# Performance work log

Measured on AMD Instinct MI355X. Metric: run time of the kernel, lower is better.

## Reference

```python
import jax, jax.numpy as jnp
import numpy as np

B, S, D, H, MEL = 64, 512, 512, 8, 80
HD = D // H  # head dim


def _lstm_cell(x, h, c, w_ih, w_hh, b_ih, b_hh):
    # torch gate order: i, f, g, o
    gates = x @ w_ih.T + h @ w_hh.T + b_ih + b_hh
    i, f, g, o = jnp.split(gates, 4, axis=-1)
    c = jax.nn.sigmoid(f) * c + jax.nn.sigmoid(i) * jnp.tanh(g)
    h = jax.nn.sigmoid(o) * jnp.tanh(c)
    return h, c


def setup_inputs() -> dict:
    key = jax.random.key(0)
    ks = jax.random.split(key, 24)
    s = 0.05
    inp = {"encoder_output": jax.random.normal(ks[0], (B, S, D), jnp.float32)}
    # MultiheadAttention params (torch layout: in_proj [3D, D])
    inp["attn_in_w"] = jax.random.normal(ks[1], (3 * D, D), jnp.float32) * s
    inp["attn_in_b"] = jax.random.normal(ks[2], (3 * D,), jnp.float32) * s
    inp["attn_out_w"] = jax.random.normal(ks[3], (D, D), jnp.float32) * s
    inp["attn_out_b"] = jax.random.normal(ks[4], (D,), jnp.float32) * s
    # LSTM1 (2 layers)
    names = [("l1_w_ih0", (4 * D, D)), ("l1_w_hh0", (4 * D, D)), ("l1_b_ih0", (4 * D,)), ("l1_b_hh0", (4 * D,)),
             ("l1_w_ih1", (4 * D, D)), ("l1_w_hh1", (4 * D, D)), ("l1_b_ih1", (4 * D,)), ("l1_b_hh1", (4 * D,)),
             ("l2_w_ih", (4 * D, D)), ("l2_w_hh", (4 * D, D)), ("l2_b_ih", (4 * D,)), ("l2_b_hh", (4 * D,)),
             ("proj_w", (MEL, D)), ("proj_b", (MEL,))]
    for i, (n, shp) in enumerate(names):
        inp[n] = jax.random.normal(ks[5 + i], shp, jnp.float32) * s
    return inp


def reference(encoder_output, attn_in_w, attn_in_b, attn_out_w, attn_out_b,
              l1_w_ih0, l1_w_hh0, l1_b_ih0, l1_b_hh0,
              l1_w_ih1, l1_w_hh1, l1_b_ih1, l1_b_hh1,
              l2_w_ih, l2_w_hh, l2_b_ih, l2_b_hh, proj_w, proj_b):
    b, s, d = encoder_output.shape
    max_len = s * 5
    wq, wk, wv = jnp.split(attn_in_w, 3, axis=0)
    bq, bk, bv = jnp.split(attn_in_b, 3, axis=0)
    # Precompute K, V over encoder output: [B, S, H, HD]
    K = (encoder_output @ wk.T + bk).reshape(b, s, H, HD)
    V = (encoder_output @ wv.T + bv).reshape(b, s, H, HD)
    scale = 1.0 / np.sqrt(HD)

    def attend(x):  # x: [B, D] single-token query
        q = ((x @ wq.T + bq) * scale).reshape(b, H, HD)
        scores = jnp.einsum('bhd,bshd->bhs', q, K)
        w = jax.nn.softmax(scores, axis=-1)
        ctx = jnp.einsum('bhs,bshd->bhd', w, V).reshape(b, d)
        return ctx @ attn_out_w.T + attn_out_b

    zeros = jnp.zeros((b, d), encoder_output.dtype)
    carry0 = (zeros, zeros, zeros, zeros, zeros, zeros, zeros)

    def step(carry, _):
        h10, c10, h11, c11, h2, c2, dec_in = carry
        h10, c10 = _lstm_cell(dec_in, h10, c10, l1_w_ih0, l1_w_hh0, l1_b_ih0, l1_b_hh0)
        h11, c11 = _lstm_cell(h10, h11, c11, l1_w_ih1, l1_w_hh1, l1_b_ih1, l1_b_hh1)
        attn_out = attend(h11)
        h2, c2 = _lstm_cell(attn_out, h2, c2, l2_w_ih, l2_w_hh, l2_b_ih, l2_b_hh)
        out = h2 @ proj_w.T + proj_b  # [B, MEL]
        return (h10, c10, h11, c11, h2, c2, h2), out

    _, ys = jax.lax.scan(step, carry0, None, length=max_len)
    return jnp.transpose(ys, (1, 0, 2))  # [B, max_len, MEL]
```

## Files before the change

kernel.cpp:

```cpp
#include <hip/hip_runtime.h>
#include <hip/hip_bf16.h>
#include <hip/hip_fp8.h>

#define DEV_INLINE __device__ __forceinline__

typedef __attribute__((ext_vector_type(8))) short bf16x8;
typedef __attribute__((ext_vector_type(4))) float f32x4;
typedef __attribute__((ext_vector_type(2))) float f32x2;
typedef __attribute__((ext_vector_type(4))) unsigned int u32x4;
typedef unsigned long long ull;

constexpr int Bc = 64, Sc = 512, Dc = 512, Hc = 8, HDc = 64, MELc = 80, Tc = 2560;
constexpr int OUTSTRIDE = Tc * MELc;

constexpr size_t SZ_KP8 = 64ull * 8 * 512 * 64;
constexpr size_t SZ_VP  = 64ull * 8 * 512 * 64 * 2;
constexpr size_t SZ_PL  = 128ull * 2048 * 16;
constexpr size_t OFF_KP8 = 0;
constexpr size_t OFF_VP  = OFF_KP8 + SZ_KP8;
constexpr size_t OFF_PL0 = OFF_VP + SZ_VP;
constexpr size_t OFF_PL1 = OFF_PL0 + SZ_PL;
constexpr size_t OFF_PL2 = OFF_PL1 + SZ_PL;
constexpr size_t OFF_PWQ = OFF_PL2 + SZ_PL;
constexpr size_t OFF_PP  = OFF_PWQ + 524288;
constexpr size_t OFF_BL0 = OFF_PP + 81920;
constexpr size_t OFF_BL1 = OFF_BL0 + 8192;
constexpr size_t OFF_BL2 = OFF_BL1 + 8192;
constexpr size_t OFF_B2E = OFF_BL2 + 8192;
constexpr size_t OFF_W2E = OFF_B2E + 8192;
constexpr size_t OFF_WOT = OFF_W2E + 2097152;
constexpr size_t OFF_ACT = OFF_WOT + 1048576;
constexpr size_t OFF_FLG = OFF_ACT + 524288;

constexpr unsigned DYN_LDS = 137344;

DEV_INLINE float bf2f(short s) { return __uint_as_float(((unsigned)(unsigned short)s) << 16); }
DEV_INLINE short f2bf(float f) { union { __hip_bfloat16 h; short s; } u; u.h = __float2bfloat16(f); return u.s; }
DEV_INLINE float sig_f(float x) { return 1.0f / (1.0f + __expf(-x)); }
DEV_INLINE float tanh_f(float x) {
  float ax = fabsf(x);
  float e = __expf(fminf(2.0f * ax, 80.0f));
  float r = 1.0f - 2.0f / (e + 1.0f);
  return copysignf(r, x);
}
DEV_INLINE bf16x8 cvt8(const float* p) {
  bf16x8 r;
#pragma unroll
  for (int i = 0; i < 8; ++i) r[i] = f2bf(p[i]);
  return r;
}
DEV_INLINE float fp8tof(unsigned v) {
  __hip_fp8_e4m3 t; t.__x = (__hip_fp8_storage_t)v; return (float)t;
}

template <bool HI>
DEV_INLINE f32x2 cvt2_fp8(unsigned w) {
#if defined(__has_builtin) && __has_builtin(__builtin_amdgcn_cvt_pk_f32_fp8)
  return __builtin_amdgcn_cvt_pk_f32_fp8(w, HI);
#else
  unsigned b = HI ? (w >> 16) : w;
  f32x2 r; r[0] = fp8tof(b & 0xFFu); r[1] = fp8tof((b >> 8) & 0xFFu);
  return r;
#endif
}

DEV_INLINE ull ld_dev_u64(const void* p) {
  return __hip_atomic_load((const ull*)p, __ATOMIC_RELAXED, __HIP_MEMORY_SCOPE_AGENT);
}
DEV_INLINE void st_dev_u64(void* p, ull v) {
  __hip_atomic_store((ull*)p, v, __ATOMIC_RELAXED, __HIP_MEMORY_SCOPE_AGENT);
}
DEV_INLINE bf16x8 ld_frag(const __hip_bfloat16* p) {
  union { bf16x8 v; ull u[2]; } r;
  r.u[0] = ld_dev_u64(p);
  r.u[1] = ld_dev_u64((const char*)p + 8);
  return r.v;
}

__global__ __launch_bounds__(256) void gemm_setup(const float* __restrict__ A,
                                                  const float* __restrict__ Bt,
                                                  const float* __restrict__ bias,
                                                  __hip_bfloat16* __restrict__ dst,
                                                  unsigned char* __restrict__ dst8,
                                                  int mode) {
  int tid = threadIdx.x, lane = tid & 63, wv = tid >> 6;
  int m0 = blockIdx.y * 64 + wv * 16;
  int nb = blockIdx.x * 64;
  int mrow = m0 + (lane & 15);
  int kb = (lane >> 4) * 8;
  f32x4 acc0 = {0,0,0,0}, acc1 = {0,0,0,0}, acc2 = {0,0,0,0}, acc3 = {0,0,0,0};
  const float* arow = A + (size_t)mrow * 512 + kb;
  const float* b0r = Bt + (size_t)(nb + 0 * 16 + (lane & 15)) * 512 + kb;
  const float* b1r = Bt + (size_t)(nb + 1 * 16 + (lane & 15)) * 512 + kb;
  const float* b2r = Bt + (size_t)(nb + 2 * 16 + (lane & 15)) * 512 + kb;
  const float* b3r = Bt + (size_t)(nb + 3 * 16 + (lane & 15)) * 512 + kb;
  for (int kk = 0; kk < 16; ++kk) {
    bf16x8 af = cvt8(arow + kk * 32);
    acc0 = __builtin_amdgcn_mfma_f32_16x16x32_bf16(af, cvt8(b0r + kk * 32), acc0, 0, 0, 0);
    acc1 = __builtin_amdgcn_mfma_f32_16x16x32_bf16(af, cvt8(b1r + kk * 32), acc1, 0, 0, 0);
    acc2 = __builtin_amdgcn_mfma_f32_16x16x32_bf16(af, cvt8(b2r + kk * 32), acc2, 0, 0, 0);
    acc3 = __builtin_amdgcn_mfma_f32_16x16x32_bf16(af, cvt8(b3r + kk * 32), acc3, 0, 0, 0);
  }
  int col16 = lane & 15, r0 = (lane >> 4) * 4;
  f32x4 accs[4] = {acc0, acc1, acc2, acc3};
#pragma unroll
  for (int nt = 0; nt < 4; ++nt) {
    int n = nb + nt * 16 + col16;
#pragma unroll
    for (int r = 0; r < 4; ++r) {
      int m = m0 + r0 + r;
      float v = accs[nt][r];
      if (mode == 0) {
        v += bias[n];
        int bb = m >> 9, s = m & 511, h = n >> 6, d = n & 63;
        dst[(((size_t)(bb * 8 + h) * 512 + s) * 64) + d] = __float2bfloat16(v);
      } else if (mode == 2) {
        v += bias[n];
        int bb = m >> 9, s = m & 511, h = n >> 6, d = n & 63;
        __hip_fp8_e4m3 q(v);
        dst8[(((size_t)(bb * 8 + h) * 512 + s) * 64) + d] = (unsigned char)q.__x;
      } else {
        dst[(size_t)m * 512 + n] = __float2bfloat16(v);
      }
    }
  }
}

__global__ __launch_bounds__(256) void transpose512(const float* __restrict__ in, float* __restrict__ out) {
  __shared__ float tl[32][33];
  int x = threadIdx.x & 31, ty = threadIdx.x >> 5;
  int bx = blockIdx.x * 32, by = blockIdx.y * 32;
#pragma unroll
  for (int r = 0; r < 4; ++r) tl[ty + r * 8][x] = in[(size_t)(by + ty + r * 8) * 512 + bx + x];
  __syncthreads();
#pragma unroll
  for (int r = 0; r < 4; ++r) out[(size_t)(bx + ty + r * 8) * 512 + by + x] = tl[x][ty + r * 8];
}

__global__ __launch_bounds__(256) void b2eff_k(const float* __restrict__ w2ih, const float* __restrict__ bout,
                                               const float* __restrict__ bih, const float* __restrict__ bhh,
                                               float* __restrict__ dst) {
  int g = blockIdx.x * 256 + threadIdx.x;
  float acc = bih[g] + bhh[g];
  const float* row = w2ih + (size_t)g * 512;
  for (int k = 0; k < 512; ++k) acc += row[k] * bout[k];
  dst[g] = acc;
}

__global__ __launch_bounds__(256) void pack_lstm(const float* __restrict__ lo_f32,
                                                 const __hip_bfloat16* __restrict__ lo_bf16,
                                                 const float* __restrict__ hi_f32,
                                                 const float* __restrict__ b1, const float* __restrict__ b2,
                                                 const float* __restrict__ b_pre,
                                                 __hip_bfloat16* __restrict__ dst, float* __restrict__ bias_out,
                                                 int mode) {
  int u = blockIdx.x, tid = threadIdx.x;
  for (int rep = 0; rep < 8; ++rep) {
    int slot = rep * 256 + tid;
    int kk = slot >> 6, lane = slot & 63;
    int n16 = lane & 15, gate = n16 >> 2, jj = n16 & 3;
    int srow = gate * 512 + u * 4 + jj;
    int k = kk * 32 + (lane >> 4) * 8;
    __hip_bfloat16 tmp[8];
    if (k < 512) {
      if (mode == 0) {
#pragma unroll
        for (int i = 0; i < 8; ++i) tmp[i] = __float2bfloat16(lo_f32[(size_t)srow * 512 + k + i]);
      } else {
#pragma unroll
        for (int i = 0; i < 8; ++i) tmp[i] = lo_bf16[(size_t)srow * 512 + k + i];
      }
    } else {
#pragma unroll
      for (int i = 0; i < 8; ++i) tmp[i] = __float2bfloat16(hi_f32[(size_t)srow * 512 + (k - 512) + i]);
    }
    *(uint4*)(dst + ((size_t)u * 2048 + slot) * 8) = *(uint4*)tmp;
  }
  if (tid < 16) {
    int gate = tid >> 2, jj = tid & 3;
    int srow = gate * 512 + u * 4 + jj;
    bias_out[u * 16 + tid] = (mode == 0) ? (b1[srow] + b2[srow]) : b_pre[srow];
  }
}

__global__ __launch_bounds__(256) void pack_wq(const float* __restrict__ wq, __hip_bfloat16* __restrict__ dst) {
  int h = blockIdx.x, tid = threadIdx.x;
  for (int rep = 0; rep < 16; ++rep) {
    int slot = rep * 256 + tid;
    int nt = slot >> 10, kk = (slot >> 6) & 15, lane = slot & 63;
    int srow = h * 64 + nt * 16 + (lane & 15);
    int k = kk * 32 + (lane >> 4) * 8;
    __hip_bfloat16 tmp[8];
#pragma unroll
    for (int i = 0; i < 8; ++i) tmp[i] = __float2bfloat16(wq[(size_t)srow * 512 + k + i]);
    *(uint4*)(dst + ((size_t)h * 4096 + slot) * 8) = *(uint4*)tmp;
  }
}

__global__ __launch_bounds__(256) void pack_proj(const float* __restrict__ pw, __hip_bfloat16* __restrict__ dst) {
  int u5 = blockIdx.x, tid = threadIdx.x;
  for (int rep = 0; rep < 4; ++rep) {
    int slot = rep * 256 + tid;
    int kk = slot >> 6, lane = slot & 63;
    int srow = u5 * 16 + (lane & 15);
    int k = kk * 32 + (lane >> 4) * 8;
    __hip_bfloat16 tmp[8];
#pragma unroll
    for (int i = 0; i < 8; ++i) tmp[i] = __float2bfloat16(pw[(size_t)srow * 512 + k + i]);
    *(uint4*)(dst + ((size_t)u5 * 1024 + slot) * 8) = *(uint4*)tmp;
  }
}

struct DecParams {
  const float* attn_in_b;
  const float* proj_b;
  const uint4* packL0; const uint4* packL1; const uint4* packL2;
  const float* biasL0; const float* biasL1; const float* biasL2;
  const uint4* packWq; const uint4* packP;
  const unsigned char* Kp8; const __hip_bfloat16* Vp;
  __hip_bfloat16* h10b; __hip_bfloat16* h11b; __hip_bfloat16* h2b; __hip_bfloat16* ctxb;
  ull* actbase;
  unsigned* flags;
  float* out;
};

constexpr ull WD_TICKS = 200000000ull;

DEV_INLINE void publish_flag(unsigned* flags, int wg, unsigned id, int tid) {
  __builtin_amdgcn_s_waitcnt(0);
  __syncthreads();
  if (tid == 0)
    __hip_atomic_store(&flags[wg], id, __ATOMIC_RELAXED, __HIP_MEMORY_SCOPE_AGENT);
}

DEV_INLINE bool wait_flags(unsigned* flags, int base, int count, unsigned id, int tid,
                           ull t0, int* bail) {
  if (tid < 64) {
    for (;;) {
      bool ok = true;
      for (int i = tid; i < count; i += 64)
        ok &= (__hip_atomic_load(&flags[base + i], __ATOMIC_RELAXED, __HIP_MEMORY_SCOPE_AGENT) >= id);
      if (__all(ok ? 1 : 0)) break;
      if (__builtin_amdgcn_s_memrealtime() - t0 > WD_TICKS) { if (tid == 0) *bail = 1; break; }
      __builtin_amdgcn_s_sleep(1);
    }
  }
  __syncthreads();
  if (*bail) return false;
  return true;
}

DEV_INLINE bool wait_half(unsigned* flags, int base, unsigned id, int lane, ull t0, int* sbail) {
  for (;;) {
    unsigned f = __hip_atomic_load(&flags[base + lane], __ATOMIC_RELAXED, __HIP_MEMORY_SCOPE_AGENT);
    if (__all(f >= id ? 1 : 0)) return true;
    if (__builtin_amdgcn_s_memrealtime() - t0 > WD_TICKS) { *sbail = 1; return false; }
    __builtin_amdgcn_s_sleep(1);
  }
}

DEV_INLINE void prefetch_hi(bf16x8* pf, const __hip_bfloat16* hi, int g, int lane, int wv) {
  if (wv >= 2) {
    const __hip_bfloat16* p = hi + (size_t)(g * 32 + (wv & 1) * 16 + (lane & 15)) * 512 + (lane >> 4) * 8;
#pragma unroll
    for (int kk = 0; kk < 16; ++kk) pf[kk] = ld_frag(p + kk * 32);
  }
}

DEV_INLINE bool lstm_stage(int tid, int g, int wgl,
                           const uint4* wlds, const float* bias,
                           const __hip_bfloat16* lo, const bf16x8* pf,
                           float* cstate, __hip_bfloat16* hc,
                           float* pred, ull* st64,
                           unsigned* flags, int fbase, unsigned id,
                           ull t0, int* sbail) {
  const int lane = tid & 63, wv = tid >> 6, mt = wv & 1, kh = wv >> 1;
  f32x4 acc = {0,0,0,0};
  if (kh == 0) {
    const __hip_bfloat16* pA = lo + (size_t)(g * 32 + mt * 16 + (lane & 15)) * 512 + (lane >> 4) * 8;
    if (wait_half(flags, fbase, id, lane, t0, sbail)) {
#pragma unroll
      for (int kk = 0; kk < 8; ++kk) {
        bf16x8 a = ld_frag(pA + kk * 32);
        bf16x8 b = *(const bf16x8*)(wlds + kk * 64 + lane);
        acc = __builtin_amdgcn_mfma_f32_16x16x32_bf16(a, b, acc, 0, 0, 0);
      }
      if (wait_half(flags, fbase + 64, id, lane, t0, sbail)) {
#pragma unroll
        for (int kk = 8; kk < 16; ++kk) {
          bf16x8 a = ld_frag(pA + kk * 32);
          bf16x8 b = *(const bf16x8*)(wlds + kk * 64 + lane);
          acc = __builtin_amdgcn_mfma_f32_16x16x32_bf16(a, b, acc, 0, 0, 0);
        }
      }
    }
  } else {
#pragma unroll
    for (int kk = 0; kk < 16; ++kk) {
      bf16x8 b = *(const bf16x8*)(wlds + (16 + kk) * 64 + lane);
      acc = __builtin_amdgcn_mfma_f32_16x16x32_bf16(pf[kk], b, acc, 0, 0, 0);
    }
  }
#pragma unroll
  for (int r = 0; r < 4; ++r) pred[wv * 256 + lane * 4 + r] = acc[r];
  __syncthreads();
  if (*sbail) return false;
  if (tid < 128) {
    int bl = tid >> 2, j = tid & 3;
    int mt2 = bl >> 4, qd = (bl & 15) >> 2, reg = bl & 3;
    const float* p0 = pred + mt2 * 256;
    const float* p1 = pred + (2 + mt2) * 256;
    int l0 = qd * 16;
    float gi = p0[(l0 + j) * 4 + reg]      + p1[(l0 + j) * 4 + reg]      + bias[j];
    float gf = p0[(l0 + 4 + j) * 4 + reg]  + p1[(l0 + 4 + j) * 4 + reg]  + bias[4 + j];
    float gg = p0[(l0 + 8 + j) * 4 + reg]  + p1[(l0 + 8 + j) * 4 + reg]  + bias[8 + j];
    float go = p0[(l0 + 12 + j) * 4 + reg] + p1[(l0 + 12 + j) * 4 + reg] + bias[12 + j];
    float c = cstate[tid & 127];
    c = sig_f(gf) * c + sig_f(gi) * tanh_f(gg);
    float h = sig_f(go) * tanh_f(c);
    cstate[tid & 127] = c;
    ((unsigned short*)st64)[tid] = (unsigned short)f2bf(h);
  }
  __syncthreads();
  if (tid < 32)
    st_dev_u64(hc + (size_t)(g * 32 + tid) * 512 + wgl * 4, st64[tid]);
  return true;
}

DEV_INLINE void proj_stage(int tid, int g, int n5, const uint4* wPJ, const float* proj_b,
                           const __hip_bfloat16* h2in, float* outp, float* pred) {
  const int lane = tid & 63, wv = tid >> 6, mt = wv & 1, kh = wv >> 1;
  f32x4 acc = {0,0,0,0};
  const __hip_bfloat16* pA = h2in + (size_t)(g * 32 + mt * 16 + (lane & 15)) * 512 + kh * 256 + (lane >> 4) * 8;
#pragma unroll
  for (int kk = 0; kk < 8; ++kk) {
    bf16x8 a = ld_frag(pA + kk * 32);
    bf16x8 b = *(const bf16x8*)(wPJ + (kh * 8 + kk) * 64 + lane);
    acc = __builtin_amdgcn_mfma_f32_16x16x32_bf16(a, b, acc, 0, 0, 0);
  }
#pragma unroll
  for (int r = 0; r < 4; ++r) pred[wv * 256 + lane * 4 + r] = acc[r];
  __syncthreads();
#pragma unroll
  for (int half = 0; half < 2; ++half) {
    int gx = half * 256 + tid;
    int row = gx >> 4, col = gx & 15;
    int mt2 = row >> 4, qd = (row & 15) >> 2, reg = row & 3, ln = qd * 16 + col;
    float v = pred[mt2 * 256 + ln * 4 + reg] + pred[(2 + mt2) * 256 + ln * 4 + reg] + proj_b[n5 * 16 + col];
    outp[(size_t)(g * 32 + row) * OUTSTRIDE + n5 * 16 + col] = v;
  }
  __syncthreads();
}

__global__ __launch_bounds__(256, 1) void decoder_main(DecParams P) {
  extern __shared__ char smem[];
  uint4* wL0 = (uint4*)smem;
  uint4* wL1 = wL0 + 2048;
  uint4* wL2 = wL1 + 2048;
  uint4* wPJ = wL2 + 2048;
  ull*   st64 = (ull*)(wPJ + 1024);
  float* pred = (float*)(st64 + 32);
  float* qls  = pred + 1024;
  float* sco  = qls + 1088;
  float* red  = sco + 1024;
  float* cst  = red + 2048;
  float* smx  = cst + 384;
  float* ssum = smx + 4;
  float* sinv = ssum + 4;
  int*   sbail = (int*)(sinv + 2);

  const int wg = blockIdx.x, tid = threadIdx.x;
  const int lane = tid & 63, wv = tid >> 6;
  const int g = wg >> 7;
  const int wgl = wg & 127;
  const int fbase = g * 128;
  const int hh = wgl >> 4;
  const int b0g = (wgl & 15) * 2;
  const int bblk = b0g & ~15;

  const ull t0 = __builtin_amdgcn_s_memrealtime();

  {
    const uint4* s0 = P.packL0 + (size_t)wgl * 2048;
    const uint4* s1 = P.packL1 + (size_t)wgl * 2048;
    const uint4* s2 = P.packL2 + (size_t)wgl * 2048;
    for (int i = tid; i < 2048; i += 256) { wL0[i] = s0[i]; wL1[i] = s1[i]; wL2[i] = s2[i]; }
    if (wgl < 5) { const uint4* sp = P.packP + (size_t)wgl * 1024; for (int i = tid; i < 1024; i += 256) wPJ[i] = sp[i]; }
  }
  if (tid == 0) *sbail = 0;
  if (tid < 128) { cst[tid] = 0.0f; cst[128 + tid] = 0.0f; cst[256 + tid] = 0.0f; }
  st_dev_u64(P.actbase + (size_t)wg * 256 + tid, 0ull);
  __syncthreads();
  publish_flag(P.flags, wg, 1u, tid);
  if (!wait_flags(P.flags, 0, 256, 1u, tid, t0, sbail)) goto bail;

  for (int t = 0; t < Tc; ++t) {
    const int cur = t & 1, pv = cur ^ 1;
    const unsigned idA = 4u * t + 1, idApub = 4u * t + 2, idBpub = 4u * t + 3,
                   idCpub = 4u * t + 4, idDpub = 4u * t + 5;
    __hip_bfloat16* h10c = P.h10b + cur * 32768; __hip_bfloat16* h10p = P.h10b + pv * 32768;
    __hip_bfloat16* h11c = P.h11b + cur * 32768; __hip_bfloat16* h11p = P.h11b + pv * 32768;
    __hip_bfloat16* h2c  = P.h2b  + cur * 32768; __hip_bfloat16* h2p  = P.h2b  + pv * 32768;
    __hip_bfloat16* ctxc = P.ctxb + cur * 32768;

    {
      bf16x8 pf[16];
      prefetch_hi(pf, h10p, g, lane, wv);
      if (!lstm_stage(tid, g, wgl, wL0, P.biasL0 + wgl * 16, h2p, pf, cst, h10c, pred, st64,
                      P.flags, fbase, idA, t0, sbail)) goto bail;
      publish_flag(P.flags, wg, idApub, tid);
    }
    if (wgl < 5 && t > 0)
      proj_stage(tid, g, wgl, wPJ, P.proj_b, h2p, P.out + (size_t)(t - 1) * MELc, pred);

    {
      bf16x8 pf[16];
      prefetch_hi(pf, h11p, g, lane, wv);
      if (!lstm_stage(tid, g, wgl, wL1, P.biasL1 + wgl * 16, h10c, pf, cst + 128, h11c, pred, st64,
                      P.flags, fbase, idApub, t0, sbail)) goto bail;
      publish_flag(P.flags, wg, idBpub, tid);
    }

    {
      int mrow = g * 32 + bblk + (lane & 15);
      const __hip_bfloat16* pA = h11c + (size_t)mrow * 512 + (lane >> 4) * 8;
      const uint4* pB = P.packWq + (size_t)hh * 4096 + wv * 1024;
      f32x4 acc = {0,0,0,0};
      if (wait_half(P.flags, fbase, idBpub, lane, t0, sbail)) {
#pragma unroll
        for (int kk = 0; kk < 8; ++kk) {
          bf16x8 a = ld_frag(pA + kk * 32);
          bf16x8 b = *(const bf16x8*)(pB + kk * 64 + lane);
          acc = __builtin_amdgcn_mfma_f32_16x16x32_bf16(a, b, acc, 0, 0, 0);
        }
        if (wait_half(P.flags, fbase + 64, idBpub, lane, t0, sbail)) {
#pragma unroll
          for (int kk = 8; kk < 16; ++kk) {
            bf16x8 a = ld_frag(pA + kk * 32);
            bf16x8 b = *(const bf16x8*)(pB + kk * 64 + lane);
            acc = __builtin_amdgcn_mfma_f32_16x16x32_bf16(a, b, acc, 0, 0, 0);
          }
        }
      }
      int col = lane & 15, row0 = (lane >> 4) << 2;
      int dg = wv * 16 + col;
      float bq = P.attn_in_b[hh * 64 + dg];
#pragma unroll
      for (int r = 0; r < 4; ++r) qls[(row0 + r) * 68 + dg] = (acc[r] + bq) * 0.125f;
    }
    __syncthreads();
    if (*sbail) goto bail;
    {
      int p = tid >> 7, si = tid & 127;
      int bg = g * 32 + b0g + p;
      const float* qv = qls + ((b0g & 15) + p) * 68;
      f32x4 q4[16];
#pragma unroll
      for (int i = 0; i < 16; ++i) q4[i] = *(const f32x4*)(qv + 4 * i);
      const u32x4* Kb = (const u32x4*)(P.Kp8 + (size_t)(bg * 8 + hh) * 512 * 64);
#pragma unroll
      for (int ss = 0; ss < 4; ++ss) {
        int s = si * 4 + ss;
        const u32x4* kr = Kb + s * 4;
        f32x2 acc2 = {0.0f, 0.0f};
#pragma unroll
        for (int i = 0; i < 4; ++i) {
          u32x4 kv = kr[i];
#pragma unroll
          for (int j = 0; j < 4; ++j) {
            unsigned w = kv[j];
            f32x2 c01 = cvt2_fp8<false>(w);
            f32x2 c23 = cvt2_fp8<true>(w);
            f32x4 qq = q4[i * 4 + j];
            acc2 += c01 * (f32x2){qq[0], qq[1]} + c23 * (f32x2){qq[2], qq[3]};
          }
        }
        sco[p * 512 + s] = acc2[0] + acc2[1];
      }
    }
    __syncthreads();
    {
      int p = wv >> 1, half = wv & 1;
      int idx = tid & 127;
      float mx = -1e30f;
#pragma unroll
      for (int ss = 0; ss < 4; ++ss) mx = fmaxf(mx, sco[p * 512 + idx * 4 + ss]);
#pragma unroll
      for (int off = 32; off; off >>= 1) mx = fmaxf(mx, __shfl_xor(mx, off));
      if (lane == 0) smx[p * 2 + half] = mx;
      __syncthreads();
      float m = fmaxf(smx[p * 2], smx[p * 2 + 1]);
      float sum = 0.0f;
#pragma unroll
      for (int ss = 0; ss < 4; ++ss) {
        int ix = p * 512 + idx * 4 + ss;
        float e = __expf(sco[ix] - m);
        sco[ix] = e; sum += e;
      }
#pragma unroll
      for (int off = 32; off; off >>= 1) sum += __shfl_xor(sum, off);
      if (lane == 0) ssum[p * 2 + half] = sum;
      __syncthreads();
      if (tid < 2) sinv[tid] = 1.0f / (ssum[tid * 2] + ssum[tid * 2 + 1]);
    }
    __syncthreads();
    {
      int p = wv >> 1, half = wv & 1;
      int bg = g * 32 + b0g + p;
      int sg = lane >> 3, dj = lane & 7;
      const u32x4* VbU = (const u32x4*)(P.Vp + (size_t)(bg * 8 + hh) * 512 * 64);
      f32x2 aA[4] = {{0,0},{0,0},{0,0},{0,0}};
      f32x2 aB[4] = {{0,0},{0,0},{0,0},{0,0}};
      const int s0 = half * 256 + sg;
#pragma unroll 4
      for (int it = 0; it < 16; ++it) {
        int sA = s0 + it * 8, sB = sA + 128;
        u32x4 vA = __builtin_nontemporal_load(VbU + (size_t)sA * 8 + dj);
        u32x4 vB = __builtin_nontemporal_load(VbU + (size_t)sB * 8 + dj);
        float wa = sco[p * 512 + sA], wb = sco[p * 512 + sB];
        f32x2 wA = {wa, wa}, wB = {wb, wb};
#pragma unroll
        for (int j = 0; j < 4; ++j) {
          unsigned ua = vA[j], ub = vB[j];
          f32x2 fa = { __uint_as_float(ua << 16), __uint_as_float(ua & 0xFFFF0000u) };
          f32x2 fb = { __uint_as_float(ub << 16), __uint_as_float(ub & 0xFFFF0000u) };
          aA[j] += wA * fa;
          aB[j] += wB * fb;
        }
      }
      float* rp = red + ((p * 16 + half * 8 + sg) * 64) + dj * 8;
#pragma unroll
      for (int j = 0; j < 4; ++j) {
        rp[j * 2]     = aA[j][0] + aB[j][0];
        rp[j * 2 + 1] = aA[j][1] + aB[j][1];
      }
    }
    __syncthreads();
    if (tid < 128) {
      int p = tid >> 6, d = tid & 63;
      float sacc = 0.0f;
#pragma unroll
      for (int k = 0; k < 16; ++k) sacc += red[(p * 16 + k) * 64 + d];
      sacc *= sinv[p];
      ((unsigned short*)st64)[tid] = (unsigned short)f2bf(sacc);
    }
    __syncthreads();
    if (tid < 32) {
      int p = tid >> 4, q = tid & 15;
      st_dev_u64(ctxc + (size_t)(g * 32 + b0g + p) * 512 + hh * 64 + q * 4, st64[p * 16 + q]);
    }
    publish_flag(P.flags, wg, idCpub, tid);

    {
      bf16x8 pf[16];
      prefetch_hi(pf, h2p, g, lane, wv);
      if (!lstm_stage(tid, g, wgl, wL2, P.biasL2 + wgl * 16, ctxc, pf, cst + 256, h2c, pred, st64,
                      P.flags, fbase, idCpub, t0, sbail)) goto bail;
      publish_flag(P.flags, wg, idDpub, tid);
    }
  }

  if (wgl < 5) {
    if (wait_flags(P.flags, fbase, 128, 4u * (Tc - 1) + 5, tid, t0, sbail))
      proj_stage(tid, g, wgl, wPJ, P.proj_b, P.h2b + ((Tc - 1) & 1) * 32768,
                 P.out + (size_t)(Tc - 1) * MELc, pred);
  }
  return;

bail:
  publish_flag(P.flags, wg, 0x7F000000u, tid);
}

extern "C" void kernel_launch(void* const* d_in, const int* in_sizes, int n_in,
                              void* d_out, int out_size, void* d_ws, size_t ws_size,
                              hipStream_t stream) {
  const float* enc        = (const float*)d_in[0];
  const float* attn_in_w  = (const float*)d_in[1];
  const float* attn_in_b  = (const float*)d_in[2];
  const float* attn_out_w = (const float*)d_in[3];
  const float* attn_out_b = (const float*)d_in[4];
  const float* w_ih0 = (const float*)d_in[5];
  const float* w_hh0 = (const float*)d_in[6];
  const float* b_ih0 = (const float*)d_in[7];
  const float* b_hh0 = (const float*)d_in[8];
  const float* w_ih1 = (const float*)d_in[9];
  const float* w_hh1 = (const float*)d_in[10];
  const float* b_ih1 = (const float*)d_in[11];
  const float* b_hh1 = (const float*)d_in[12];
  const float* w_ih2 = (const float*)d_in[13];
  const float* w_hh2 = (const float*)d_in[14];
  const float* b_ih2 = (const float*)d_in[15];
  const float* b_hh2 = (const float*)d_in[16];
  const float* proj_w = (const float*)d_in[17];
  const float* proj_b = (const float*)d_in[18];

  char* ws = (char*)d_ws;
  unsigned char*  Kp8 = (unsigned char*)(ws + OFF_KP8);
  __hip_bfloat16* Vp  = (__hip_bfloat16*)(ws + OFF_VP);
  __hip_bfloat16* pl0 = (__hip_bfloat16*)(ws + OFF_PL0);
  __hip_bfloat16* pl1 = (__hip_bfloat16*)(ws + OFF_PL1);
  __hip_bfloat16* pl2 = (__hip_bfloat16*)(ws + OFF_PL2);
  __hip_bfloat16* pwq = (__hip_bfloat16*)(ws + OFF_PWQ);
  __hip_bfloat16* pp  = (__hip_bfloat16*)(ws + OFF_PP);
  float* bl0 = (float*)(ws + OFF_BL0);
  float* bl1 = (float*)(ws + OFF_BL1);
  float* bl2 = (float*)(ws + OFF_BL2);
  float* b2e = (float*)(ws + OFF_B2E);
  __hip_bfloat16* w2e = (__hip_bfloat16*)(ws + OFF_W2E);
  float* wot = (float*)(ws + OFF_WOT);
  char* act  = ws + OFF_ACT;
  unsigned* flags = (unsigned*)(ws + OFF_FLG);

  hipMemsetAsync(flags, 0, 4096, stream);

  gemm_setup<<<dim3(8, 512), 256, 0, stream>>>(enc, attn_in_w + 512 * 512, attn_in_b + 512, nullptr, Kp8, 2);
  gemm_setup<<<dim3(8, 512), 256, 0, stream>>>(enc, attn_in_w + 1024 * 512, attn_in_b + 1024, Vp, nullptr, 0);
  transpose512<<<dim3(16, 16), 256, 0, stream>>>(attn_out_w, wot);
  gemm_setup<<<dim3(8, 32), 256, 0, stream>>>(w_ih2, wot, nullptr, w2e, nullptr, 1);
  b2eff_k<<<8, 256, 0, stream>>>(w_ih2, attn_out_b, b_ih2, b_hh2, b2e);
  pack_lstm<<<128, 256, 0, stream>>>(w_ih0, nullptr, w_hh0, b_ih0, b_hh0, nullptr, pl0, bl0, 0);
  pack_lstm<<<128, 256, 0, stream>>>(w_ih1, nullptr, w_hh1, b_ih1, b_hh1, nullptr, pl1, bl1, 0);
  pack_lstm<<<128, 256, 0, stream>>>(nullptr, w2e, w_hh2, nullptr, nullptr, b2e, pl2, bl2, 1);
  pack_wq<<<8, 256, 0, stream>>>(attn_in_w, pwq);
  pack_proj<<<5, 256, 0, stream>>>(proj_w, pp);

  DecParams p;
  p.attn_in_b = attn_in_b;
  p.proj_b = proj_b;
  p.packL0 = (const uint4*)pl0; p.packL1 = (const uint4*)pl1; p.packL2 = (const uint4*)pl2;
  p.biasL0 = bl0; p.biasL1 = bl1; p.biasL2 = bl2;
  p.packWq = (const uint4*)pwq; p.packP = (const uint4*)pp;
  p.Kp8 = Kp8; p.Vp = Vp;
  p.h10b = (__hip_bfloat16*)(act + 0);
  p.h11b = (__hip_bfloat16*)(act + 131072);
  p.h2b  = (__hip_bfloat16*)(act + 262144);
  p.ctxb = (__hip_bfloat16*)(act + 393216);
  p.actbase = (ull*)act;
  p.flags = flags;
  p.out = (float*)d_out;

  (void)hipFuncSetAttribute((const void*)decoder_main,
                            hipFuncAttributeMaxDynamicSharedMemorySize, DYN_LDS);
  decoder_main<<<dim3(256), dim3(256), DYN_LDS, stream>>>(p);
}
```

Before: 111.6 ms.

## Spread mel projection across all workgroups and drop LDS-resident proj weights

Replaces the MFMA projection, which ran only on the first 5 workgroups of each group, with a per-output dot product spread over all 128 workgroups of a group. Each wave computes one (batch, mel) output by reading fp32 proj weights straight from global memory and reducing with a wave shuffle. This removes the load imbalance where a few workgroups did extra work each timestep on the critical path, and frees LDS. The change also swaps the V loads from nontemporal 128-bit loads to pairs of device-scope 64-bit loads, and adds a duplicated flag poll in wait_half.

```diff
diff --git a/kernel.cpp b/kernel.cpp
--- a/kernel.cpp
+++ b/kernel.cpp
@@ -32,7 +32,7 @@
 constexpr size_t OFF_ACT = OFF_WOT + 1048576;
 constexpr size_t OFF_FLG = OFF_ACT + 524288;
 
-constexpr unsigned DYN_LDS = 137344;
+constexpr unsigned DYN_LDS = 121088;
 
 DEV_INLINE float bf2f(short s) { return __uint_as_float(((unsigned)(unsigned short)s) << 16); }
 DEV_INLINE short f2bf(float f) { union { __hip_bfloat16 h; short s; } u; u.h = __float2bfloat16(f); return u.s; }
@@ -197,26 +197,13 @@
   }
 }
 
-__global__ __launch_bounds__(256) void pack_proj(const float* __restrict__ pw, __hip_bfloat16* __restrict__ dst) {
-  int u5 = blockIdx.x, tid = threadIdx.x;
-  for (int rep = 0; rep < 4; ++rep) {
-    int slot = rep * 256 + tid;
-    int kk = slot >> 6, lane = slot & 63;
-    int srow = u5 * 16 + (lane & 15);
-    int k = kk * 32 + (lane >> 4) * 8;
-    __hip_bfloat16 tmp[8];
-#pragma unroll
-    for (int i = 0; i < 8; ++i) tmp[i] = __float2bfloat16(pw[(size_t)srow * 512 + k + i]);
-    *(uint4*)(dst + ((size_t)u5 * 1024 + slot) * 8) = *(uint4*)tmp;
-  }
-}
-
 struct DecParams {
   const float* attn_in_b;
   const float* proj_b;
+  const float* proj_w;
   const uint4* packL0; const uint4* packL1; const uint4* packL2;
   const float* biasL0; const float* biasL1; const float* biasL2;
-  const uint4* packWq; const uint4* packP;
+  const uint4* packWq;
   const unsigned char* Kp8; const __hip_bfloat16* Vp;
   __hip_bfloat16* h10b; __hip_bfloat16* h11b; __hip_bfloat16* h2b; __hip_bfloat16* ctxb;
   ull* actbase;
@@ -252,8 +239,10 @@
 
 DEV_INLINE bool wait_half(unsigned* flags, int base, unsigned id, int lane, ull t0, int* sbail) {
   for (;;) {
-    unsigned f = __hip_atomic_load(&flags[base + lane], __ATOMIC_RELAXED, __HIP_MEMORY_SCOPE_AGENT);
-    if (__all(f >= id ? 1 : 0)) return true;
+    unsigned f0 = __hip_atomic_load(&flags[base + lane], __ATOMIC_RELAXED, __HIP_MEMORY_SCOPE_AGENT);
+    unsigned f1 = __hip_atomic_load(&flags[base + lane], __ATOMIC_RELAXED, __HIP_MEMORY_SCOPE_AGENT);
+    if (__all(f0 >= id ? 1 : 0)) return true;
+    if (__all(f1 >= id ? 1 : 0)) return true;
     if (__builtin_amdgcn_s_memrealtime() - t0 > WD_TICKS) { *sbail = 1; return false; }
     __builtin_amdgcn_s_sleep(1);
   }
@@ -327,29 +316,22 @@
   return true;
 }
 
-DEV_INLINE void proj_stage(int tid, int g, int n5, const uint4* wPJ, const float* proj_b,
-                           const __hip_bfloat16* h2in, float* outp, float* pred) {
-  const int lane = tid & 63, wv = tid >> 6, mt = wv & 1, kh = wv >> 1;
-  f32x4 acc = {0,0,0,0};
-  const __hip_bfloat16* pA = h2in + (size_t)(g * 32 + mt * 16 + (lane & 15)) * 512 + kh * 256 + (lane >> 4) * 8;
-#pragma unroll
-  for (int kk = 0; kk < 8; ++kk) {
-    bf16x8 a = ld_frag(pA + kk * 32);
-    bf16x8 b = *(const bf16x8*)(wPJ + (kh * 8 + kk) * 64 + lane);
-    acc = __builtin_amdgcn_mfma_f32_16x16x32_bf16(a, b, acc, 0, 0, 0);
-  }
-#pragma unroll
-  for (int r = 0; r < 4; ++r) pred[wv * 256 + lane * 4 + r] = acc[r];
-  __syncthreads();
-#pragma unroll
-  for (int half = 0; half < 2; ++half) {
-    int gx = half * 256 + tid;
-    int row = gx >> 4, col = gx & 15;
-    int mt2 = row >> 4, qd = (row & 15) >> 2, reg = row & 3, ln = qd * 16 + col;
-    float v = pred[mt2 * 256 + ln * 4 + reg] + pred[(2 + mt2) * 256 + ln * 4 + reg] + proj_b[n5 * 16 + col];
-    outp[(size_t)(g * 32 + row) * OUTSTRIDE + n5 * 16 + col] = v;
-  }
-  __syncthreads();
+DEV_INLINE void proj_spread(int tid, int g, int wgl, const float* pw, const float* pb,
+                            const __hip_bfloat16* h2in, float* outp) {
+  const int lane = tid & 63, pr = tid >> 6;
+#pragma unroll
+  for (int r = 0; r < 5; ++r) {
+    int P = wgl * 20 + r * 4 + pr;
+    int b = P / 80, m = P - b * 80;
+    bf16x8 hv = ld_frag(h2in + (size_t)(g * 32 + b) * 512 + lane * 8);
+    const f32x4* w4 = (const f32x4*)(pw + (size_t)m * 512 + lane * 8);
+    f32x4 wa = w4[0], wb = w4[1];
+    float acc = bf2f(hv[0]) * wa[0] + bf2f(hv[1]) * wa[1] + bf2f(hv[2]) * wa[2] + bf2f(hv[3]) * wa[3]
+              + bf2f(hv[4]) * wb[0] + bf2f(hv[5]) * wb[1] + bf2f(hv[6]) * wb[2] + bf2f(hv[7]) * wb[3];
+#pragma unroll
+    for (int off = 32; off; off >>= 1) acc += __shfl_xor(acc, off);
+    if (lane == 0) outp[(size_t)(g * 32 + b) * OUTSTRIDE + m] = acc + pb[m];
+  }
 }
 
 __global__ __launch_bounds__(256, 1) void decoder_main(DecParams P) {
@@ -357,8 +339,7 @@
   uint4* wL0 = (uint4*)smem;
   uint4* wL1 = wL0 + 2048;
   uint4* wL2 = wL1 + 2048;
-  uint4* wPJ = wL2 + 2048;
-  ull*   st64 = (ull*)(wPJ + 1024);
+  ull*   st64 = (ull*)(wL2 + 2048);
   float* pred = (float*)(st64 + 32);
   float* qls  = pred + 1024;
   float* sco  = qls + 1088;
@@ -385,7 +366,6 @@
     const uint4* s1 = P.packL1 + (size_t)wgl * 2048;
     const uint4* s2 = P.packL2 + (size_t)wgl * 2048;
     for (int i = tid; i < 2048; i += 256) { wL0[i] = s0[i]; wL1[i] = s1[i]; wL2[i] = s2[i]; }
-    if (wgl < 5) { const uint4* sp = P.packP + (size_t)wgl * 1024; for (int i = tid; i < 1024; i += 256) wPJ[i] = sp[i]; }
   }
   if (tid == 0) *sbail = 0;
   if (tid < 128) { cst[tid] = 0.0f; cst[128 + tid] = 0.0f; cst[256 + tid] = 0.0f; }
@@ -410,8 +390,8 @@
                       P.flags, fbase, idA, t0, sbail)) goto bail;
       publish_flag(P.flags, wg, idApub, tid);
     }
-    if (wgl < 5 && t > 0)
-      proj_stage(tid, g, wgl, wPJ, P.proj_b, h2p, P.out + (size_t)(t - 1) * MELc, pred);
+    if (t > 0)
+      proj_spread(tid, g, wgl, P.proj_w, P.proj_b, h2p, P.out + (size_t)(t - 1) * MELc);
 
     {
       bf16x8 pf[16];
@@ -508,22 +488,25 @@
       int p = wv >> 1, half = wv & 1;
       int bg = g * 32 + b0g + p;
       int sg = lane >> 3, dj = lane & 7;
-      const u32x4* VbU = (const u32x4*)(P.Vp + (size_t)(bg * 8 + hh) * 512 * 64);
+      const char* Vb = (const char*)(P.Vp + (size_t)(bg * 8 + hh) * 512 * 64);
       f32x2 aA[4] = {{0,0},{0,0},{0,0},{0,0}};
       f32x2 aB[4] = {{0,0},{0,0},{0,0},{0,0}};
       const int s0 = half * 256 + sg;
 #pragma unroll 4
       for (int it = 0; it < 16; ++it) {
         int sA = s0 + it * 8, sB = sA + 128;
-        u32x4 vA = __builtin_nontemporal_load(VbU + (size_t)sA * 8 + dj);
-        u32x4 vB = __builtin_nontemporal_load(VbU + (size_t)sB * 8 + dj);
+        const char* pa = Vb + (size_t)sA * 128 + dj * 16;
+        const char* pq = Vb + (size_t)sB * 128 + dj * 16;
+        ull a0 = ld_dev_u64(pa), a1 = ld_dev_u64(pa + 8);
+        ull b0 = ld_dev_u64(pq), b1 = ld_dev_u64(pq + 8);
         float wa = sco[p * 512 + sA], wb = sco[p * 512 + sB];
         f32x2 wA = {wa, wa}, wB = {wb, wb};
+        unsigned va[4] = {(unsigned)a0, (unsigned)(a0 >> 32), (unsigned)a1, (unsigned)(a1 >> 32)};
+        unsigned vb[4] = {(unsigned)b0, (unsigned)(b0 >> 32), (unsigned)b1, (unsigned)(b1 >> 32)};
 #pragma unroll
         for (int j = 0; j < 4; ++j) {
-          unsigned ua = vA[j], ub = vB[j];
-          f32x2 fa = { __uint_as_float(ua << 16), __uint_as_float(ua & 0xFFFF0000u) };
-          f32x2 fb = { __uint_as_float(ub << 16), __uint_as_float(ub & 0xFFFF0000u) };
+          f32x2 fa = { __uint_as_float(va[j] << 16), __uint_as_float(va[j] & 0xFFFF0000u) };
+          f32x2 fb = { __uint_as_float(vb[j] << 16), __uint_as_float(vb[j] & 0xFFFF0000u) };
           aA[j] += wA * fa;
           aB[j] += wB * fb;
         }
@@ -560,11 +543,9 @@
     }
   }
 
-  if (wgl < 5) {
-    if (wait_flags(P.flags, fbase, 128, 4u * (Tc - 1) + 5, tid, t0, sbail))
-      proj_stage(tid, g, wgl, wPJ, P.proj_b, P.h2b + ((Tc - 1) & 1) * 32768,
-                 P.out + (size_t)(Tc - 1) * MELc, pred);
-  }
+  if (wait_flags(P.flags, fbase, 128, 4u * (Tc - 1) + 5, tid, t0, sbail))
+    proj_spread(tid, g, wgl, P.proj_w, P.proj_b, P.h2b + ((Tc - 1) & 1) * 32768,
+                P.out + (size_t)(Tc - 1) * MELc);
   return;
 
 bail:
@@ -601,7 +582,6 @@
   __hip_bfloat16* pl1 = (__hip_bfloat16*)(ws + OFF_PL1);
   __hip_bfloat16* pl2 = (__hip_bfloat16*)(ws + OFF_PL2);
   __hip_bfloat16* pwq = (__hip_bfloat16*)(ws + OFF_PWQ);
-  __hip_bfloat16* pp  = (__hip_bfloat16*)(ws + OFF_PP);
   float* bl0 = (float*)(ws + OFF_BL0);
   float* bl1 = (float*)(ws + OFF_BL1);
   float* bl2 = (float*)(ws + OFF_BL2);
@@ -622,14 +602,14 @@
   pack_lstm<<<128, 256, 0, stream>>>(w_ih1, nullptr, w_hh1, b_ih1, b_hh1, nullptr, pl1, bl1, 0);
   pack_lstm<<<128, 256, 0, stream>>>(nullptr, w2e, w_hh2, nullptr, nullptr, b2e, pl2, bl2, 1);
   pack_wq<<<8, 256, 0, stream>>>(attn_in_w, pwq);
-  pack_proj<<<5, 256, 0, stream>>>(proj_w, pp);
 
   DecParams p;
   p.attn_in_b = attn_in_b;
   p.proj_b = proj_b;
+  p.proj_w = proj_w;
   p.packL0 = (const uint4*)pl0; p.packL1 = (const uint4*)pl1; p.packL2 = (const uint4*)pl2;
   p.biasL0 = bl0; p.biasL1 = bl1; p.biasL2 = bl2;
-  p.packWq = (const uint4*)pwq; p.packP = (const uint4*)pp;
+  p.packWq = (const uint4*)pwq;
   p.Kp8 = Kp8; p.Vp = Vp;
   p.h10b = (__hip_bfloat16*)(act + 0);
   p.h11b = (__hip_bfloat16*)(act + 131072);
```

Measured after the change: 107.4 ms. -3.7%, faster.
